# Performance work log

Hardware: AMD Instinct MI355X
Metric: run time of the kernel (lower is better)

The kernel has to match this reference:

```python
import jax, jax.numpy as jnp
import numpy as np


def _pool_mat(N, pn):
    # F.interpolate(mode='area') == adaptive_avg_pool1d: output i averages
    # input indices [floor(i*N/pn), ceil((i+1)*N/pn))
    W = np.zeros((pn, N), dtype=np.float32)
    for i in range(pn):
        s = (i * N) // pn
        e = -((-(i + 1) * N) // pn)  # ceil((i+1)*N/pn)
        W[i, s:e] = 1.0 / (e - s)
    return W


def _up_mat(pn, N):
    # F.interpolate(mode='linear', align_corners=False) from length pn to N
    W = np.zeros((N, pn), dtype=np.float32)
    scale = pn / N
    for j in range(N):
        pos = max((j + 0.5) * scale - 0.5, 0.0)
        i0 = min(int(np.floor(pos)), pn - 1)
        i1 = min(i0 + 1, pn - 1)
        frac = pos - i0
        W[j, i0] += 1.0 - frac
        W[j, i1] += frac
    return W


def setup_inputs() -> dict:
    key = jax.random.key(0)
    k1, k2 = jax.random.split(key)
    B, N, C, K = 512, 16, 256, 8192
    f = jax.random.normal(k1, (B, N, C), dtype=jnp.float32)
    # original init: uniform(-1/K, 1/K)
    emb = jax.random.uniform(k2, (K, C), dtype=jnp.float32, minval=-1.0 / K, maxval=1.0 / K)
    return {"f": f, "emb": emb}


def reference(f, emb):
    B, N, C = f.shape
    fT = jnp.transpose(f, (0, 2, 1))            # [B, C, N]
    f_ng = jax.lax.stop_gradient(fT)
    emb_ng = jax.lax.stop_gradient(emb)
    e_sq = jnp.sum(emb_ng * emb_ng, axis=1)     # [K]
    f_rest = f_ng
    f_hat = jnp.zeros_like(f_ng)
    commit = jnp.float32(0.0)
    qlat = jnp.float32(0.0)
    for pn in range(1, N + 1):
        rest_bcn = jax.lax.stop_gradient(f_rest)
        if pn < N:
            Wp = jnp.asarray(_pool_mat(N, pn))             # [pn, N]
            rest = jnp.einsum('pn,bcn->bpc', Wp, rest_bcn).reshape(-1, C)
        else:
            rest = jnp.transpose(rest_bcn, (0, 2, 1)).reshape(-1, C)
        # squared euclidean distances [B*pn, K]
        d = jnp.sum(rest * rest, axis=1, keepdims=True) + e_sq - 2.0 * (rest @ emb_ng.T)
        idx = jnp.argmin(d, axis=1).reshape(B, pn)
        h = jnp.transpose(emb[idx], (0, 2, 1))             # [B, C, pn]
        if pn < N:
            Wu = jnp.asarray(_up_mat(pn, N))               # [N, pn]
            h = jnp.einsum('np,bcp->bcn', Wu, h)
        f_hat = f_hat + h
        f_rest = f_rest - h
        commit = commit + 0.25 * jnp.mean((jax.lax.stop_gradient(f_hat) - fT) ** 2)
        qlat = qlat + jnp.mean((f_hat - f_ng) ** 2)
    commit = commit / N
    qlat = qlat / N
    # straight-through estimator
    f_hat_out = jax.lax.stop_gradient(f_hat) - f_ng + fT
    return jnp.transpose(f_hat_out, (0, 2, 1)), commit, qlat
```

## Files before the change

kernel.cpp:

```cpp
#include <hip/hip_runtime.h>
#include <math.h>

#define BB 512
#define NN 16
#define CC 256
#define KK 8192
#define BNC (BB*NN*CC)

typedef unsigned short u16;
typedef __attribute__((ext_vector_type(8))) short bf16x8;
typedef __attribute__((ext_vector_type(4))) float f32x4;

__device__ __forceinline__ u16 f2bf(float x) {
    unsigned u = __float_as_uint(x);
    unsigned r = (u + 0x7fffu + ((u >> 16) & 1u)) >> 16;
    return (u16)r;
}

__device__ __forceinline__ void gl2lds16(const void* g, void* l) {
    __builtin_amdgcn_global_load_lds(
        (const __attribute__((address_space(1))) void*)g,
        (__attribute__((address_space(3))) void*)l,
        16, 0, 0);
}

__device__ __forceinline__ void gl2lds4(const void* g, void* l) {
    __builtin_amdgcn_global_load_lds(
        (const __attribute__((address_space(1))) void*)g,
        (__attribute__((address_space(3))) void*)l,
        4, 0, 0);
}

__global__ void esq_kernel(const float* __restrict__ emb, float* __restrict__ e_sq) {
    int gid  = blockIdx.x * blockDim.x + threadIdx.x;
    int wave = gid >> 6;
    int lane = gid & 63;
    const float4 v = *(const float4*)(emb + (size_t)wave * CC + lane * 4);
    float s = v.x*v.x + v.y*v.y + v.z*v.z + v.w*v.w;
    #pragma unroll
    for (int m = 32; m >= 1; m >>= 1) s += __shfl_xor(s, m, 64);
    if (lane == 0) e_sq[wave] = 0.5f * s;
}

__global__ void cvt_emb_kernel(const float* __restrict__ emb, u16* __restrict__ out) {
    int gid = blockIdx.x * blockDim.x + threadIdx.x;
    float4 v = ((const float4*)emb)[gid];
    ushort4 o;
    o.x = f2bf(-v.x); o.y = f2bf(-v.y); o.z = f2bf(-v.z); o.w = f2bf(-v.w);
    ((ushort4*)out)[gid] = o;
}

__global__ void init_pool_kernel(const float* __restrict__ f,
                                 u16* __restrict__ rest_bf) {
    int b = blockIdx.x;
    int c = threadIdx.x;
    const float* base = f + (size_t)b * NN * CC + c;
    float acc = 0.f;
    #pragma unroll
    for (int n = 0; n < NN; ++n) acc += base[(size_t)n * CC];
    rest_bf[(size_t)b * CC + c] = f2bf(acc * (1.0f / 16.0f));
}

__device__ __forceinline__ unsigned long long shfl_xor_u64(unsigned long long v, int m) {
    unsigned lo = (unsigned)v, hi = (unsigned)(v >> 32);
    lo = __shfl_xor(lo, m, 64);
    hi = __shfl_xor(hi, m, 64);
    return ((unsigned long long)hi << 32) | lo;
}

__global__ __launch_bounds__(256, 2) void dist_mfma_kernel(
        const u16* __restrict__ A, const u16* __restrict__ Bm,
        const float* __restrict__ e_sq,
        unsigned long long* __restrict__ packed, int cpb) {
    __shared__ __align__(16) u16 sC[32768];
    __shared__ __align__(16) float sE[512];
    const int tid = threadIdx.x;
    const int w = tid >> 6, l = tid & 63;
    const int r0 = blockIdx.x * 256;
    const int c0 = blockIdx.y * cpb;
    const int nch = cpb >> 3;
    const int ncb2 = cpb >> 6;
    const int arow = l & 15;
    const int aq   = l >> 4;

    bf16x8 bf[4][8];
    {
        const u16* fb = A + (((size_t)(r0 + w * 64 + arow)) << 8) + aq * 8;
        #pragma unroll
        for (int j = 0; j < 4; ++j)
            #pragma unroll
            for (int kc = 0; kc < 8; ++kc)
                bf[j][kc] = *(const bf16x8*)(fb + (j << 12) + (kc << 5));
    }

    for (int n = tid; n < cpb; n += 256)
        gl2lds4(e_sq + c0 + n, (char*)sE + (size_t)(n - l) * 4);

    const int crel = w * 16 + (l >> 2);
    const int g = (l & 3) ^ ((l >> 3) & 3);
    const u16* Pb = Bm + (((size_t)(c0 + crel)) << 8) + g * 8;

    #define STAGEC(t_) { \
        int tt_ = (t_); if (tt_ >= nch) tt_ = nch - 1; \
        const u16* s_ = Pb + (((size_t)(tt_ >> 3)) << 14) + ((tt_ & 7) << 5); \
        gl2lds16(s_, (char*)sC + (((t_) & 3) << 12) + (w << 10)); }

    STAGEC(0) STAGEC(1) STAGEC(2)

    const int gx = aq ^ ((arow >> 1) & 3);
    float bestd[4];
    int   bestk[4];
    #pragma unroll
    for (int j = 0; j < 4; ++j) { bestd[j] = 1e30f; bestk[j] = 0; }

    for (int cb = 0; cb < ncb2; ++cb) {
        f32x4 acc[4][4];
        #pragma unroll
        for (int kc = 0; kc < 8; ++kc) {
            const int t = cb * 8 + kc;
            asm volatile("s_waitcnt vmcnt(2)" ::: "memory");
            __builtin_amdgcn_s_barrier();
            STAGEC(t + 3)
            if (kc == 0) {
                #pragma unroll
                for (int i = 0; i < 4; ++i) {
                    f32x4 ev = *(const f32x4*)(sE + cb * 64 + i * 16 + (aq << 2));
                    #pragma unroll
                    for (int j = 0; j < 4; ++j) acc[i][j] = ev;
                }
            }
            bf16x8 cf[4];
            const u16* cbp = sC + ((t & 3) << 11);
            #pragma unroll
            for (int i = 0; i < 4; ++i)
                cf[i] = *(const bf16x8*)(cbp + ((i * 16 + arow) << 5) + (gx << 3));
            __builtin_amdgcn_s_setprio(1);
            #pragma unroll
            for (int i = 0; i < 4; ++i)
                #pragma unroll
                for (int j = 0; j < 4; ++j)
                    acc[i][j] = __builtin_amdgcn_mfma_f32_16x16x32_bf16(
                                    cf[i], bf[j][kc], acc[i][j], 0, 0, 0);
            __builtin_amdgcn_s_setprio(0);
            asm volatile("s_waitcnt lgkmcnt(0)" ::: "memory");
        }

        #pragma unroll
        for (int i = 0; i < 4; ++i)
            #pragma unroll
            for (int r = 0; r < 4; ++r) {
                const int k = c0 + cb * 64 + i * 16 + (aq << 2) + r;
                #pragma unroll
                for (int j = 0; j < 4; ++j) {
                    const float d = acc[i][j][r];
                    if (d < bestd[j]) { bestd[j] = d; bestk[j] = k; }
                }
            }
    }
    #undef STAGEC

    #pragma unroll
    for (int j = 0; j < 4; ++j) {
        unsigned u = __float_as_uint(bestd[j]);
        u = (u & 0x80000000u) ? ~u : (u | 0x80000000u);
        unsigned long long p = ((unsigned long long)u << 32) | (unsigned)bestk[j];
        unsigned long long o = shfl_xor_u64(p, 16);
        if (o < p) p = o;
        o = shfl_xor_u64(p, 32);
        if (o < p) p = o;
        if (aq == 0)
            atomicMin(&packed[r0 + w * 64 + j * 16 + arow], p);
    }
}

__global__ void update_pool_kernel(const float* __restrict__ f,
                                   const float* __restrict__ emb,
                                   const unsigned long long* __restrict__ packed,
                                   float* __restrict__ f_rest,
                                   float* __restrict__ f_hat,
                                   float* __restrict__ slots,
                                   u16* __restrict__ rest_bf, int pn) {
    int b = blockIdx.x;
    int c = threadIdx.x;
    __shared__ int sk[NN];
    __shared__ float red[4];
    if (threadIdx.x < pn)
        sk[threadIdx.x] = (int)(unsigned)(packed[b * pn + threadIdx.x] & 0xffffffffull);
    __syncthreads();

    float fr[NN];
    float acc_sq = 0.f;
    #pragma unroll
    for (int n = 0; n < NN; ++n) {
        double pos = (n + 0.5) * ((double)pn / 16.0) - 0.5;
        if (pos < 0.0) pos = 0.0;
        int i0 = (int)floor(pos);
        if (i0 > pn - 1) i0 = pn - 1;
        int i1 = i0 + 1;
        if (i1 > pn - 1) i1 = pn - 1;
        double frac = pos - (double)i0;
        float w1 = (float)frac;
        float w0 = (float)(1.0 - frac);
        float h = w0 * emb[(size_t)sk[i0] * CC + c] + w1 * emb[(size_t)sk[i1] * CC + c];
        size_t off = ((size_t)b * NN + n) * CC + c;
        float fh = f_hat[off] + h;
        f_hat[off] = fh;
        float fre = f_rest[off] - h;
        f_rest[off] = fre;
        fr[n] = fre;
        float diff = fh - f[off];
        acc_sq += diff * diff;
    }

    int wv = threadIdx.x >> 6, ln = threadIdx.x & 63;
    #pragma unroll
    for (int m = 32; m >= 1; m >>= 1) acc_sq += __shfl_xor(acc_sq, m, 64);
    if (ln == 0) red[wv] = acc_sq;

    int pn2 = pn + 1;
    if (pn < NN) {
        for (int p = 0; p < pn2; ++p) {
            int s = (p * NN) / pn2;
            int e = ((p + 1) * NN + pn2 - 1) / pn2;
            float v = 0.f;
            for (int n = s; n < e; ++n) v += fr[n];
            v *= 1.0f / (float)(e - s);
            rest_bf[((size_t)(b * pn2 + p)) * CC + c] = f2bf(v);
        }
    }
    __syncthreads();
    if (threadIdx.x == 0)
        atomicAdd(&slots[b & 255], (red[0] + red[1]) + (red[2] + red[3]));
}

__global__ void final_kernel(const float* __restrict__ slots, float* __restrict__ out_scalars) {
    float v = slots[threadIdx.x];
    #pragma unroll
    for (int m = 32; m >= 1; m >>= 1) v += __shfl_xor(v, m, 64);
    __shared__ float red[4];
    int wv = threadIdx.x >> 6, ln = threadIdx.x & 63;
    if (ln == 0) red[wv] = v;
    __syncthreads();
    if (threadIdx.x == 0) {
        float S = (red[0] + red[1]) + (red[2] + red[3]);
        float qlat = S / (float)BNC / (float)NN;
        out_scalars[0] = 0.25f * qlat;
        out_scalars[1] = qlat;
    }
}

extern "C" void kernel_launch(void* const* d_in, const int* in_sizes, int n_in,
                              void* d_out, int out_size, void* d_ws, size_t ws_size,
                              hipStream_t stream) {
    (void)in_sizes; (void)n_in; (void)out_size; (void)ws_size;
    const float* f   = (const float*)d_in[0];
    const float* emb = (const float*)d_in[1];
    float* out = (float*)d_out;

    float* ws      = (float*)d_ws;
    float* f_rest  = ws;
    float* r2_pad  = f_rest + BNC;
    float* e_sq    = r2_pad + BB * NN;
    float* slots   = e_sq + KK;
    unsigned long long* packed_all = (unsigned long long*)(slots + 256);
    u16* rest_bf = (u16*)(packed_all + (size_t)BB * 136);
    u16* emb_bf  = rest_bf + (size_t)BB * NN * CC;

    float* f_hat = out;

    hipMemsetAsync(out, 0, (size_t)BNC * sizeof(float), stream);
    hipMemcpyAsync(f_rest, f, (size_t)BNC * sizeof(float), hipMemcpyDeviceToDevice, stream);
    hipMemsetAsync(slots, 0, 256 * sizeof(float), stream);
    hipMemsetAsync(packed_all, 0xFF, (size_t)BB * 136 * sizeof(unsigned long long), stream);
    esq_kernel<<<KK / 4, 256, 0, stream>>>(emb, e_sq);
    cvt_emb_kernel<<<KK * CC / 4 / 256, 256, 0, stream>>>(emb, emb_bf);
    init_pool_kernel<<<BB, 256, 0, stream>>>(f, rest_bf);

    static const int splits_tab[17] =
        {0,128,64,64,32,32,32,32,16,16,16,16,16,16,16,16,16};

    for (int pn = 1; pn <= NN; ++pn) {
        unsigned long long* packed = packed_all + (size_t)BB * (pn * (pn - 1) / 2);
        int splits = splits_tab[pn];
        int cpb = KK / splits;
        dim3 grid(BB * pn / 256, splits);
        dist_mfma_kernel<<<grid, 256, 0, stream>>>(rest_bf, emb_bf, e_sq, packed, cpb);
        update_pool_kernel<<<BB, 256, 0, stream>>>(f, emb, packed, f_rest, f_hat,
                                                   slots, rest_bf, pn);
    }
    final_kernel<<<1, 256, 0, stream>>>(slots, out + BNC);
}
```

Before: 787.9 us.

## Stage whole codebook blocks with double buffering and raise split counts

The distance kernel used to stream codebook chunks one 8-element-deep slice at a time through a 4-slot ring, with a barrier before every MFMA step. It now loads an entire 64-code block (8 slices) into one of two LDS buffers while the other is being computed on, so there is one barrier per block instead of per slice. The per-pn split table is also raised so each phase launches more blocks over the codebook. This cuts synchronisation overhead and adds parallelism, but it needs more LDS per block (the full 64KB buffer) and hides less latency inside a block, and the larger splits mean more atomicMin traffic.

New measurement: 722.4 us. -8.3%, faster.

```diff
diff --git a/kernel.cpp b/kernel.cpp
--- a/kernel.cpp
+++ b/kernel.cpp
@@ -78,7 +78,6 @@
     const int w = tid >> 6, l = tid & 63;
     const int r0 = blockIdx.x * 256;
     const int c0 = blockIdx.y * cpb;
-    const int nch = cpb >> 3;
     const int ncb2 = cpb >> 6;
     const int arow = l & 15;
     const int aq   = l >> 4;
@@ -100,12 +99,14 @@
     const int g = (l & 3) ^ ((l >> 3) & 3);
     const u16* Pb = Bm + (((size_t)(c0 + crel)) << 8) + g * 8;
 
-    #define STAGEC(t_) { \
-        int tt_ = (t_); if (tt_ >= nch) tt_ = nch - 1; \
-        const u16* s_ = Pb + (((size_t)(tt_ >> 3)) << 14) + ((tt_ & 7) << 5); \
-        gl2lds16(s_, (char*)sC + (((t_) & 3) << 12) + (w << 10)); }
-
-    STAGEC(0) STAGEC(1) STAGEC(2)
+    #define STAGE_CB(cb_) { \
+        const u16* s0_ = Pb + ((size_t)(cb_) << 14); \
+        char* d0_ = (char*)sC + (((cb_) & 1) << 15) + (w << 10); \
+        _Pragma("unroll") \
+        for (int c_ = 0; c_ < 8; ++c_) \
+            gl2lds16(s0_ + (c_ << 5), d0_ + (c_ << 12)); }
+
+    STAGE_CB(0)
 
     const int gx = aq ^ ((arow >> 1) & 3);
     float bestd[4];
@@ -113,24 +114,26 @@
     #pragma unroll
     for (int j = 0; j < 4; ++j) { bestd[j] = 1e30f; bestk[j] = 0; }
 
+    asm volatile("s_waitcnt vmcnt(0)" ::: "memory");
+    __builtin_amdgcn_s_barrier();
+    asm volatile("" ::: "memory");
+
     for (int cb = 0; cb < ncb2; ++cb) {
+        if (cb + 1 < ncb2) STAGE_CB(cb + 1)
+
         f32x4 acc[4][4];
         #pragma unroll
-        for (int kc = 0; kc < 8; ++kc) {
-            const int t = cb * 8 + kc;
-            asm volatile("s_waitcnt vmcnt(2)" ::: "memory");
-            __builtin_amdgcn_s_barrier();
-            STAGEC(t + 3)
-            if (kc == 0) {
-                #pragma unroll
-                for (int i = 0; i < 4; ++i) {
-                    f32x4 ev = *(const f32x4*)(sE + cb * 64 + i * 16 + (aq << 2));
-                    #pragma unroll
-                    for (int j = 0; j < 4; ++j) acc[i][j] = ev;
-                }
-            }
+        for (int i = 0; i < 4; ++i) {
+            f32x4 ev = *(const f32x4*)(sE + cb * 64 + i * 16 + (aq << 2));
+            #pragma unroll
+            for (int j = 0; j < 4; ++j) acc[i][j] = ev;
+        }
+
+        const u16* bufp = sC + ((cb & 1) << 14);
+        #pragma unroll
+        for (int c = 0; c < 8; ++c) {
             bf16x8 cf[4];
-            const u16* cbp = sC + ((t & 3) << 11);
+            const u16* cbp = bufp + (c << 11);
             #pragma unroll
             for (int i = 0; i < 4; ++i)
                 cf[i] = *(const bf16x8*)(cbp + ((i * 16 + arow) << 5) + (gx << 3));
@@ -140,9 +143,8 @@
                 #pragma unroll
                 for (int j = 0; j < 4; ++j)
                     acc[i][j] = __builtin_amdgcn_mfma_f32_16x16x32_bf16(
-                                    cf[i], bf[j][kc], acc[i][j], 0, 0, 0);
+                                    cf[i], bf[j][c], acc[i][j], 0, 0, 0);
             __builtin_amdgcn_s_setprio(0);
-            asm volatile("s_waitcnt lgkmcnt(0)" ::: "memory");
         }
 
         #pragma unroll
@@ -156,8 +158,12 @@
                     if (d < bestd[j]) { bestd[j] = d; bestk[j] = k; }
                 }
             }
-    }
-    #undef STAGEC
+
+        asm volatile("s_waitcnt vmcnt(0) lgkmcnt(0)" ::: "memory");
+        __builtin_amdgcn_s_barrier();
+        asm volatile("" ::: "memory");
+    }
+    #undef STAGE_CB
 
     #pragma unroll
     for (int j = 0; j < 4; ++j) {
@@ -277,7 +283,7 @@
     init_pool_kernel<<<BB, 256, 0, stream>>>(f, rest_bf);
 
     static const int splits_tab[17] =
-        {0,128,64,64,32,32,32,32,16,16,16,16,16,16,16,16,16};
+        {0,128,128,128,64,64,64,64,32,32,32,32,32,32,32,32,16};
 
     for (int pn = 1; pn <= NN; ++pn) {
         unsigned long long* packed = packed_all + (size_t)BB * (pn * (pn - 1) / 2);
```
